# Kernel tuning notes

Measured on AMD Instinct MI355X. Metric: run time of the kernel, lower is better.

## Reference

```python
import jax, jax.numpy as jnp
import numpy as np
import math

FEAT_DIM = 256
QUERY_DIM = 256
HIDDEN = 64
OUT_DIM = 256
HEADS = 8


def setup_inputs() -> dict:
    key = jax.random.key(0)
    ks = jax.random.split(key, 10)
    B, NQ, NKV = 2, 2048, 2048
    s_q = 1.0 / math.sqrt(QUERY_DIM)
    s_f = 1.0 / math.sqrt(FEAT_DIM)
    s_o = 1.0 / math.sqrt(HIDDEN * HEADS)
    return {
        "feat": jax.random.normal(ks[0], (B, NKV, FEAT_DIM), jnp.float32),
        "query": jax.random.normal(ks[1], (B, NQ, QUERY_DIM), jnp.float32),
        # stacked per-head weights (each head has its own Linear in torch)
        "Wq": jax.random.uniform(ks[2], (HEADS, QUERY_DIM, HIDDEN), jnp.float32, -s_q, s_q),
        "bq": jax.random.uniform(ks[3], (HEADS, HIDDEN), jnp.float32, -s_q, s_q),
        "Wk": jax.random.uniform(ks[4], (HEADS, FEAT_DIM, HIDDEN), jnp.float32, -s_f, s_f),
        "bk": jax.random.uniform(ks[5], (HEADS, HIDDEN), jnp.float32, -s_f, s_f),
        "Wv": jax.random.uniform(ks[6], (HEADS, FEAT_DIM, HIDDEN), jnp.float32, -s_f, s_f),
        "bv": jax.random.uniform(ks[7], (HEADS, HIDDEN), jnp.float32, -s_f, s_f),
        "Wo": jax.random.uniform(ks[8], (HEADS * HIDDEN, OUT_DIM), jnp.float32, -s_o, s_o),
        "bo": jax.random.uniform(ks[9], (OUT_DIM,), jnp.float32, -s_o, s_o),
    }


def reference(feat, query, Wq, bq, Wk, bk, Wv, bv, Wo, bo):
    # Per-head projections, vectorized over the head axis h.
    # q: [B, H, Nq, E]; k, v: [B, H, Nkv, E]
    q = jnp.einsum("bnd,hde->bhne", query, Wq) + bq[None, :, None, :]
    k = jnp.einsum("bnd,hde->bhne", feat, Wk) + bk[None, :, None, :]
    v = jnp.einsum("bnd,hde->bhne", feat, Wv) + bv[None, :, None, :]
    scale = 1.0 / math.sqrt(HIDDEN)
    scores = jnp.einsum("bhqe,bhke->bhqk", q, k) * scale  # [B, H, Nq, Nkv]
    prob = jax.nn.softmax(scores, axis=-1)
    # dropout p=0.0 (eval) -> identity
    heads = jnp.einsum("bhqk,bhke->bhqe", prob, v)  # [B, H, Nq, E]
    # concat heads in order (head 0 first) then output projection
    B, H, NQ, E = heads.shape
    cat = heads.transpose(0, 2, 1, 3).reshape(B, NQ, H * E)
    return cat @ Wo + bo
```

## Files before the change

### kernel.cpp

```cpp
#include <hip/hip_runtime.h>
#include <hip/hip_bf16.h>

typedef unsigned short u16;
typedef __attribute__((ext_vector_type(8))) short short8;
typedef __attribute__((ext_vector_type(4))) float f32x4;
typedef __attribute__((ext_vector_type(16))) float f32x16;
typedef __attribute__((ext_vector_type(2))) int v2i;

#define HEADS 8
#define HID 64
#define QSCALE 0.18033688011112042f

__device__ inline u16 f2bf(float f){
    unsigned u = __float_as_uint(f);
    unsigned r = (u + 0x7fffu + ((u >> 16) & 1u)) >> 16;
    return (u16)r;
}

__device__ inline int cvtpk(float lo, float hi){
    int r;
    asm("v_cvt_pk_bf16_f32 %0, %1, %2" : "=v"(r) : "v"(lo), "v"(hi));
    return r;
}

__device__ inline float exp2fast(float x){
    float r;
    asm("v_exp_f32 %0, %1" : "=v"(r) : "v"(x));
    return r;
}

__device__ inline float xhalf_max(float x){
    v2i r = __builtin_amdgcn_permlane32_swap(__float_as_int(x), __float_as_int(x), false, false);
    return fmaxf(__int_as_float(r.x), __int_as_float(r.y));
}
__device__ inline float xhalf_sum(float x){
    v2i r = __builtin_amdgcn_permlane32_swap(__float_as_int(x), __float_as_int(x), false, false);
    return __int_as_float(r.x) + __int_as_float(r.y);
}

__global__ __launch_bounds__(256) void prep_weights(
    const float* __restrict__ query, const float* __restrict__ feat,
    const float* __restrict__ Wq, const float* __restrict__ Wk,
    const float* __restrict__ Wv, const float* __restrict__ Wo,
    u16* __restrict__ Xbq, u16* __restrict__ Xbf,
    u16* __restrict__ WqT, u16* __restrict__ WkT, u16* __restrict__ WvT,
    u16* __restrict__ WoT)
{
    int id = blockIdx.x * 256 + threadIdx.x;
    if (id < 262144) {
        const float* src = (id < 131072) ? query : feat;
        u16* dst = (id < 131072) ? Xbq : Xbf;
        int r = (id < 131072) ? id : id - 131072;
        float4 a = *reinterpret_cast<const float4*>(&src[r * 8]);
        float4 b = *reinterpret_cast<const float4*>(&src[r * 8 + 4]);
        uint4 s;
        s.x = (unsigned)cvtpk(a.x, a.y);
        s.y = (unsigned)cvtpk(a.z, a.w);
        s.z = (unsigned)cvtpk(b.x, b.y);
        s.w = (unsigned)cvtpk(b.z, b.w);
        *reinterpret_cast<uint4*>(&dst[r * 8]) = s;
    } else if (id < 655360) {
        int id2 = id - 262144;
        int w = id2 / 131072;
        int r = id2 % 131072;
        int c = r >> 8;
        int d = r & 255;
        const float* W = (w == 0) ? Wq : (w == 1 ? Wk : Wv);
        u16* WT = (w == 0) ? WqT : (w == 1 ? WkT : WvT);
        WT[c * 256 + d] = f2bf(W[(c >> 6) * (256 * 64) + d * 64 + (c & 63)]);
    } else {
        int r = id - 655360;
        int o = r >> 9;
        int k = r & 511;
        WoT[o * 512 + k] = f2bf(Wo[k * 256 + o]);
    }
}

__global__ __launch_bounds__(256) void proj_kernel(
    const u16* __restrict__ Xbq, const u16* __restrict__ Xbf,
    const u16* __restrict__ WqT, const u16* __restrict__ WkT, const u16* __restrict__ WvT,
    const float* __restrict__ bq, const float* __restrict__ bk, const float* __restrict__ bv,
    u16* __restrict__ Qb, u16* __restrict__ KVf)
{
    int which = blockIdx.z;
    const u16* Xb = (which == 0) ? Xbq : Xbf;
    const u16* WT = (which == 0) ? WqT : (which == 1 ? WkT : WvT);
    const float* bias = (which == 0) ? bq : (which == 1 ? bk : bv);
    int m0 = blockIdx.x * 64;
    int n0 = blockIdx.y * 64;
    int t = threadIdx.x;
    int lane = t & 63, w = t >> 6;
    int l15 = lane & 15, kof = (lane >> 4) * 8;

    __shared__ __align__(16) u16 lA[64][72];
    __shared__ __align__(16) u16 lB[64][72];

    f32x4 acc[4] = {};
    for (int kt = 0; kt < 256; kt += 64) {
        #pragma unroll
        for (int i = 0; i < 2; i++) {
            int lin = t + i * 256;
            int row = lin >> 3, c8 = (lin & 7) * 8;
            *reinterpret_cast<uint4*>(&lA[row][c8]) =
                *reinterpret_cast<const uint4*>(&Xb[(m0 + row) * 256 + kt + c8]);
            *reinterpret_cast<uint4*>(&lB[row][c8]) =
                *reinterpret_cast<const uint4*>(&WT[(n0 + row) * 256 + kt + c8]);
        }
        __syncthreads();
        #pragma unroll
        for (int ks = 0; ks < 2; ks++) {
            short8 a = *reinterpret_cast<const short8*>(&lA[w * 16 + l15][ks * 32 + kof]);
            #pragma unroll
            for (int nt = 0; nt < 4; nt++) {
                short8 b = *reinterpret_cast<const short8*>(&lB[nt * 16 + l15][ks * 32 + kof]);
                acc[nt] = __builtin_amdgcn_mfma_f32_16x16x32_bf16(a, b, acc[nt], 0, 0, 0);
            }
        }
        __syncthreads();
    }
    #pragma unroll
    for (int nt = 0; nt < 4; nt++) {
        #pragma unroll
        for (int i = 0; i < 4; i++) {
            int mrow = m0 + w * 16 + (lane >> 4) * 4 + i;
            int col = n0 + nt * 16 + l15;
            float val = acc[nt][i] + bias[col];
            int b_ = mrow >> 11, n = mrow & 2047;
            int h = col >> 6, e = col & 63;
            int bh = b_ * 8 + h;
            if (which == 0) {
                Qb[(bh * 2048 + n) * 64 + e] = f2bf(val * QSCALE);
            } else {
                int tile = n >> 6, nl = n & 63;
                size_t base = ((size_t)(bh * 32 + tile)) * 8192;
                size_t idx;
                if (which == 1) {
                    int reg  = ((nl >> 5) << 2) | (e >> 4);
                    int ln   = (nl & 31) | (((e >> 3) & 1) << 5);
                    idx = base + reg * 512 + ln * 8 + (e & 7);
                } else {
                    int reg  = ((e >> 5) << 2) | (nl >> 4);
                    int ln   = (e & 31) | (((nl >> 3) & 1) << 5);
                    idx = base + 4096 + reg * 512 + ln * 8 + (nl & 7);
                }
                KVf[idx] = f2bf(val);
            }
        }
    }
}

__global__ __launch_bounds__(256, 2) void attn_kernel(
    const u16* __restrict__ Qb, const u16* __restrict__ KVf, u16* __restrict__ cat)
{
    int lb = blockIdx.x;
    int chunk = lb >> 4;
    int bh = ((lb & 7) << 1) | ((lb >> 3) & 1);
    int b_ = bh >> 3, head = bh & 7;
    int t = threadIdx.x, lane = t & 63, w = t >> 6;
    int l31 = lane & 31, hh = lane >> 5;
    int sp = w >> 1, kvh = w & 1;
    int q0 = chunk * 64 + sp * 32;

    __shared__ __align__(16) u16 smem[32768];
    u16* tiles = smem;
    float* Ol = (float*)smem;
    float* Ml = (float*)(smem + 16896);
    float* Ll = (float*)(smem + 17152);

    const u16* KVfB = KVf + ((size_t)(bh * 32 + kvh * 16)) * 8192;

    short8 qf[4];
    {
        const u16* qp = Qb + (bh * 2048 + q0 + l31) * 64 + hh * 8;
        #pragma unroll
        for (int kc = 0; kc < 4; kc++)
            qf[kc] = *reinterpret_cast<const short8*>(qp + kc * 16);
    }

    f32x16 o0 = {}, o1 = {};
    float mrun = -1e30f, lrun = 0.0f;

#define PACKP(sb, base, out) {                                              \
        int A0 = cvtpk(sb[base+0], sb[base+1]);                             \
        int B0 = cvtpk(sb[base+4], sb[base+5]);                             \
        v2i r0 = __builtin_amdgcn_permlane32_swap(A0, B0, false, false);    \
        int A1 = cvtpk(sb[base+2], sb[base+3]);                             \
        int B1 = cvtpk(sb[base+6], sb[base+7]);                             \
        v2i r1 = __builtin_amdgcn_permlane32_swap(A1, B1, false, false);    \
        union { int i[4]; short8 s; } uu;                                   \
        uu.i[0] = r0.x; uu.i[1] = r1.x; uu.i[2] = r0.y; uu.i[3] = r1.y;     \
        out = uu.s; }

    auto stage = [&](int buf, int tile) {
        const u16* gsrc = KVfB + (size_t)tile * 8192;
        u16* ldst = tiles + (kvh * 2 + buf) * 8192;
        #pragma unroll
        for (int c = 0; c < 8; c++) {
            int off = (sp * 8 + c) * 512 + lane * 8;
            __builtin_amdgcn_global_load_lds(
                (const __attribute__((address_space(1))) unsigned int*)(const void*)(gsrc + off),
                (__attribute__((address_space(3))) unsigned int*)(void*)(ldst + off),
                16, 0, 0);
        }
    };

    stage(0, 0);
    asm volatile("s_waitcnt vmcnt(0)" ::: "memory");
    __syncthreads();

    int cur = 0;
    for (int tt = 0; tt < 16; tt++) {
        if (tt < 15) stage(cur ^ 1, tt + 1);

        const u16* kbase = tiles + (kvh * 2 + cur) * 8192;
        short8 kf[8], vf[8];
        #pragma unroll
        for (int r = 0; r < 8; r++)
            kf[r] = *reinterpret_cast<const short8*>(kbase + r * 512 + lane * 8);
        #pragma unroll
        for (int r = 0; r < 8; r++)
            vf[r] = *reinterpret_cast<const short8*>(kbase + 4096 + r * 512 + lane * 8);

        f32x16 s0 = {}, s1 = {};
        __builtin_amdgcn_s_setprio(1);
        #pragma unroll
        for (int kc = 0; kc < 4; kc++)
            s0 = __builtin_amdgcn_mfma_f32_32x32x16_bf16(kf[kc], qf[kc], s0, 0, 0, 0);
        #pragma unroll
        for (int kc = 0; kc < 4; kc++)
            s1 = __builtin_amdgcn_mfma_f32_32x32x16_bf16(kf[4 + kc], qf[kc], s1, 0, 0, 0);
        __builtin_amdgcn_s_setprio(0);

        float pm[8];
        #pragma unroll
        for (int r = 0; r < 8; r++)
            pm[r] = fmaxf(fmaxf(s0[r], s0[r + 8]), fmaxf(s1[r], s1[r + 8]));
        #pragma unroll
        for (int st = 4; st > 0; st >>= 1)
            #pragma unroll
            for (int r = 0; r < 8; r++) if (r < st) pm[r] = fmaxf(pm[r], pm[r + st]);
        float pmax = xhalf_max(pm[0]);
        if (__any(pmax > mrun + 6.0f)) {
            float mnew = fmaxf(mrun, pmax);
            float corr = exp2fast(mrun - mnew);
            mrun = mnew;
            lrun *= corr;
            #pragma unroll
            for (int r = 0; r < 16; r++) { o0[r] *= corr; o1[r] *= corr; }
        }
        float ac[4] = {0.f, 0.f, 0.f, 0.f};
        #pragma unroll
        for (int r = 0; r < 16; r++) {
            float p0 = exp2fast(s0[r] - mrun);
            float p1 = exp2fast(s1[r] - mrun);
            s0[r] = p0; s1[r] = p1;
            ac[r & 3] += p0 + p1;
        }
        float lsum = (ac[0] + ac[1]) + (ac[2] + ac[3]);
        lrun += xhalf_sum(lsum);

        short8 pf[4];
        PACKP(s0, 0, pf[0]); PACKP(s0, 8, pf[1]);
        PACKP(s1, 0, pf[2]); PACKP(s1, 8, pf[3]);

        __builtin_amdgcn_s_setprio(1);
        #pragma unroll
        for (int c = 0; c < 4; c++) {
            o0 = __builtin_amdgcn_mfma_f32_32x32x16_bf16(vf[c],     pf[c], o0, 0, 0, 0);
            o1 = __builtin_amdgcn_mfma_f32_32x32x16_bf16(vf[4 + c], pf[c], o1, 0, 0, 0);
        }
        __builtin_amdgcn_s_setprio(0);

        asm volatile("s_waitcnt vmcnt(0)" ::: "memory");
        __syncthreads();
        cur ^= 1;
    }

    #pragma unroll
    for (int eb = 0; eb < 2; eb++) {
        #pragma unroll
        for (int r = 0; r < 16; r++) {
            int d = eb * 32 + (r & 3) + 8 * (r >> 2) + 4 * hh;
            Ol[(w * 64 + d) * 33 + l31] = eb ? o1[r] : o0[r];
        }
    }
    if (hh == 0) { Ml[w * 32 + l31] = mrun; Ll[w * 32 + l31] = lrun; }
    __syncthreads();

    {
        int msp = t >> 7;
        int tt2 = t & 127;
        int q = tt2 >> 2;
        int d0 = (tt2 & 3) * 16;
        int wA = msp * 2, wB = msp * 2 + 1;
        float mA = Ml[wA * 32 + q], mB = Ml[wB * 32 + q];
        float ms = fmaxf(mA, mB);
        float scA = exp2fast(mA - ms), scB = exp2fast(mB - ms);
        float lsum = Ll[wA * 32 + q] * scA + Ll[wB * 32 + q] * scB;
        float linv = 1.0f / lsum;
        float vv[16];
        #pragma unroll
        for (int j = 0; j < 16; j++)
            vv[j] = (Ol[(wA * 64 + d0 + j) * 33 + q] * scA +
                     Ol[(wB * 64 + d0 + j) * 33 + q] * scB) * linv;
        uint4 st0, st1;
        st0.x = (unsigned)cvtpk(vv[0],  vv[1]);
        st0.y = (unsigned)cvtpk(vv[2],  vv[3]);
        st0.z = (unsigned)cvtpk(vv[4],  vv[5]);
        st0.w = (unsigned)cvtpk(vv[6],  vv[7]);
        st1.x = (unsigned)cvtpk(vv[8],  vv[9]);
        st1.y = (unsigned)cvtpk(vv[10], vv[11]);
        st1.z = (unsigned)cvtpk(vv[12], vv[13]);
        st1.w = (unsigned)cvtpk(vv[14], vv[15]);
        u16* crow = cat + (b_ * 2048 + chunk * 64 + msp * 32 + q) * 512 + head * 64 + d0;
        *reinterpret_cast<uint4*>(crow) = st0;
        *reinterpret_cast<uint4*>(crow + 8) = st1;
    }
#undef PACKP
}

__global__ __launch_bounds__(256) void outproj_kernel(
    const u16* __restrict__ cat, const u16* __restrict__ WoT,
    const float* __restrict__ bo, float* __restrict__ out)
{
    int m0 = blockIdx.x * 64, n0 = blockIdx.y * 64;
    int t = threadIdx.x, lane = t & 63, w = t >> 6;
    int l15 = lane & 15, kof = (lane >> 4) * 8;

    __shared__ __align__(16) u16 lA[64][72];
    __shared__ __align__(16) u16 lB[64][72];

    f32x4 acc[4] = {};
    for (int kt = 0; kt < 512; kt += 64) {
        #pragma unroll
        for (int i = 0; i < 2; i++) {
            int lin = t + i * 256;
            int row = lin >> 3, c8 = (lin & 7) * 8;
            *reinterpret_cast<uint4*>(&lA[row][c8]) =
                *reinterpret_cast<const uint4*>(&cat[(m0 + row) * 512 + kt + c8]);
            *reinterpret_cast<uint4*>(&lB[row][c8]) =
                *reinterpret_cast<const uint4*>(&WoT[(n0 + row) * 512 + kt + c8]);
        }
        __syncthreads();
        #pragma unroll
        for (int ks = 0; ks < 2; ks++) {
            short8 a = *reinterpret_cast<const short8*>(&lA[w * 16 + l15][ks * 32 + kof]);
            #pragma unroll
            for (int nt = 0; nt < 4; nt++) {
                short8 b = *reinterpret_cast<const short8*>(&lB[nt * 16 + l15][ks * 32 + kof]);
                acc[nt] = __builtin_amdgcn_mfma_f32_16x16x32_bf16(a, b, acc[nt], 0, 0, 0);
            }
        }
        __syncthreads();
    }
    #pragma unroll
    for (int i = 0; i < 4; i++) {
        int mrow = m0 + w * 16 + (lane >> 4) * 4 + i;
        #pragma unroll
        for (int nt = 0; nt < 4; nt++) {
            int col = n0 + nt * 16 + l15;
            out[mrow * 256 + col] = acc[nt][i] + bo[col];
        }
    }
}

extern "C" void kernel_launch(void* const* d_in, const int* in_sizes, int n_in,
                              void* d_out, int out_size, void* d_ws, size_t ws_size,
                              hipStream_t stream) {
    const float* feat  = (const float*)d_in[0];
    const float* query = (const float*)d_in[1];
    const float* Wq = (const float*)d_in[2];
    const float* bq = (const float*)d_in[3];
    const float* Wk = (const float*)d_in[4];
    const float* bk = (const float*)d_in[5];
    const float* Wv = (const float*)d_in[6];
    const float* bv = (const float*)d_in[7];
    const float* Wo = (const float*)d_in[8];
    const float* bo = (const float*)d_in[9];
    float* out = (float*)d_out;

    char* ws = (char*)d_ws;
    u16* WqT = (u16*)(ws + 0);
    u16* WkT = (u16*)(ws + 262144);
    u16* WvT = (u16*)(ws + 524288);
    u16* WoT = (u16*)(ws + 786432);
    u16* Qb  = (u16*)(ws + 1048576);
    u16* KVf = (u16*)(ws + 5242880);
    u16* cat = (u16*)(ws + 13631488);
    u16* Xbq = (u16*)(ws + 17825792);
    u16* Xbf = (u16*)(ws + 19922944);

    hipLaunchKernelGGL(prep_weights, dim3(3072), dim3(256), 0, stream,
                       query, feat, Wq, Wk, Wv, Wo, Xbq, Xbf, WqT, WkT, WvT, WoT);
    hipLaunchKernelGGL(proj_kernel, dim3(64, 8, 3), dim3(256), 0, stream,
                       Xbq, Xbf, WqT, WkT, WvT, bq, bk, bv, Qb, KVf);
    hipLaunchKernelGGL(attn_kernel, dim3(512), dim3(256), 0, stream,
                       Qb, KVf, cat);
    hipLaunchKernelGGL(outproj_kernel, dim3(64, 4), dim3(256), 0, stream,
                       cat, WoT, bo, out);
}
```

Baseline: 59.36 us.

## Load K/V fragments directly from global into registers with register double-buffering

Removes the LDS staging of K/V tiles through global_load_lds and the per-tile barrier. Each wave now loads its K and V fragments straight from global memory into registers, using two register sets so the next tile's loads are in flight while the current tile is computed. Shared memory shrinks to just the epilogue reduction buffers, which may allow higher occupancy. The cost is more VGPR pressure and reliance on L2 for K/V reuse across the two waves sharing a KV half, plus one redundant wrapped load on the last iteration.

After: 58.35 us. Within noise of the previous version (-1.7%).

```diff
diff --git a/kernel.cpp b/kernel.cpp
--- a/kernel.cpp
+++ b/kernel.cpp
@@ -161,11 +161,9 @@
     int sp = w >> 1, kvh = w & 1;
     int q0 = chunk * 64 + sp * 32;
 
-    __shared__ __align__(16) u16 smem[32768];
-    u16* tiles = smem;
-    float* Ol = (float*)smem;
-    float* Ml = (float*)(smem + 16896);
-    float* Ll = (float*)(smem + 17152);
+    __shared__ float Ol[4][64][33];
+    __shared__ float Ml[4][32];
+    __shared__ float Ll[4][32];
 
     const u16* KVfB = KVf + ((size_t)(bh * 32 + kvh * 16)) * 8192;
 
@@ -191,36 +189,17 @@
         uu.i[0] = r0.x; uu.i[1] = r1.x; uu.i[2] = r0.y; uu.i[3] = r1.y;     \
         out = uu.s; }
 
-    auto stage = [&](int buf, int tile) {
-        const u16* gsrc = KVfB + (size_t)tile * 8192;
-        u16* ldst = tiles + (kvh * 2 + buf) * 8192;
-        #pragma unroll
-        for (int c = 0; c < 8; c++) {
-            int off = (sp * 8 + c) * 512 + lane * 8;
-            __builtin_amdgcn_global_load_lds(
-                (const __attribute__((address_space(1))) unsigned int*)(const void*)(gsrc + off),
-                (__attribute__((address_space(3))) unsigned int*)(void*)(ldst + off),
-                16, 0, 0);
-        }
+    auto loadKV = [&](short8 (&kf)[8], short8 (&vf)[8], int ttt) {
+        const u16* p = KVfB + (size_t)ttt * 8192 + lane * 8;
+        #pragma unroll
+        for (int r = 0; r < 8; r++)
+            kf[r] = *reinterpret_cast<const short8*>(p + r * 512);
+        #pragma unroll
+        for (int r = 0; r < 8; r++)
+            vf[r] = *reinterpret_cast<const short8*>(p + 4096 + r * 512);
     };
 
-    stage(0, 0);
-    asm volatile("s_waitcnt vmcnt(0)" ::: "memory");
-    __syncthreads();
-
-    int cur = 0;
-    for (int tt = 0; tt < 16; tt++) {
-        if (tt < 15) stage(cur ^ 1, tt + 1);
-
-        const u16* kbase = tiles + (kvh * 2 + cur) * 8192;
-        short8 kf[8], vf[8];
-        #pragma unroll
-        for (int r = 0; r < 8; r++)
-            kf[r] = *reinterpret_cast<const short8*>(kbase + r * 512 + lane * 8);
-        #pragma unroll
-        for (int r = 0; r < 8; r++)
-            vf[r] = *reinterpret_cast<const short8*>(kbase + 4096 + r * 512 + lane * 8);
-
+    auto compute = [&](short8 (&kf)[8], short8 (&vf)[8]) {
         f32x16 s0 = {}, s1 = {};
         __builtin_amdgcn_s_setprio(1);
         #pragma unroll
@@ -270,10 +249,17 @@
             o1 = __builtin_amdgcn_mfma_f32_32x32x16_bf16(vf[4 + c], pf[c], o1, 0, 0, 0);
         }
         __builtin_amdgcn_s_setprio(0);
-
-        asm volatile("s_waitcnt vmcnt(0)" ::: "memory");
-        __syncthreads();
-        cur ^= 1;
+    };
+
+    short8 ka[8], va[8], kb2[8], vb2[8];
+    loadKV(ka, va, 0);
+    for (int tt = 0; tt < 16; tt += 2) {
+        loadKV(kb2, vb2, tt + 1);
+        __builtin_amdgcn_sched_barrier(0);
+        compute(ka, va);
+        loadKV(ka, va, (tt + 2) & 15);
+        __builtin_amdgcn_sched_barrier(0);
+        compute(kb2, vb2);
     }
 
     #pragma unroll
@@ -281,10 +267,10 @@
         #pragma unroll
         for (int r = 0; r < 16; r++) {
             int d = eb * 32 + (r & 3) + 8 * (r >> 2) + 4 * hh;
-            Ol[(w * 64 + d) * 33 + l31] = eb ? o1[r] : o0[r];
-        }
-    }
-    if (hh == 0) { Ml[w * 32 + l31] = mrun; Ll[w * 32 + l31] = lrun; }
+            Ol[w][d][l31] = eb ? o1[r] : o0[r];
+        }
+    }
+    if (hh == 0) { Ml[w][l31] = mrun; Ll[w][l31] = lrun; }
     __syncthreads();
 
     {
@@ -293,16 +279,15 @@
         int q = tt2 >> 2;
         int d0 = (tt2 & 3) * 16;
         int wA = msp * 2, wB = msp * 2 + 1;
-        float mA = Ml[wA * 32 + q], mB = Ml[wB * 32 + q];
+        float mA = Ml[wA][q], mB = Ml[wB][q];
         float ms = fmaxf(mA, mB);
         float scA = exp2fast(mA - ms), scB = exp2fast(mB - ms);
-        float lsum = Ll[wA * 32 + q] * scA + Ll[wB * 32 + q] * scB;
+        float lsum = Ll[wA][q] * scA + Ll[wB][q] * scB;
         float linv = 1.0f / lsum;
         float vv[16];
         #pragma unroll
         for (int j = 0; j < 16; j++)
-            vv[j] = (Ol[(wA * 64 + d0 + j) * 33 + q] * scA +
-                     Ol[(wB * 64 + d0 + j) * 33 + q] * scB) * linv;
+            vv[j] = (Ol[wA][d0 + j][q] * scA + Ol[wB][d0 + j][q] * scB) * linv;
         uint4 st0, st1;
         st0.x = (unsigned)cvtpk(vv[0],  vv[1]);
         st0.y = (unsigned)cvtpk(vv[2],  vv[3]);
```
